# Optimization experiments

Measured on AMD Instinct MI355X. Metric: run time of the kernel, lower is better.

Reference implementation:

```python
import jax, jax.numpy as jnp
import numpy as np

B, L = 8192, 8192

def setup_inputs() -> dict:
    key = jax.random.key(0)
    ka, kb = jax.random.split(key)
    a = jax.random.normal(ka, (B, L), dtype=jnp.float32)
    b = jax.random.normal(kb, (B, L), dtype=jnp.float32)
    return {"a": a, "b": b}

def reference(a, b):
    # Original: (a[:, None, :] * b[:, :, None]).sum(-1)
    # out[n, i] = sum_j a[n, j] * b[n, i] = b[n, i] * sum_j a[n, j]
    # Algebraically identical, avoids the O(B*L*L) intermediate.
    return b * jnp.sum(a, axis=-1, keepdims=True)
```

## Files before the change

kernel.cpp:

```cpp
#include <hip/hip_runtime.h>


constexpr int L = 8192;
constexpr int BLOCK = 256;
constexpr int VEC_PER_THREAD = L / 4 / BLOCK;

__global__ __launch_bounds__(BLOCK) void outer_row_scale_kernel(
    const float* __restrict__ a,
    const float* __restrict__ b,
    float* __restrict__ out) {
    const size_t row = blockIdx.x;
    const float4* __restrict__ arow = reinterpret_cast<const float4*>(a + row * L);
    const float4* __restrict__ brow = reinterpret_cast<const float4*>(b + row * L);
    float4* __restrict__ orow = reinterpret_cast<float4*>(out + row * L);

    const int tid = threadIdx.x;

    float s = 0.0f;
    float4 va[VEC_PER_THREAD];
#pragma unroll
    for (int k = 0; k < VEC_PER_THREAD; ++k) {
        va[k] = arow[tid + k * BLOCK];
    }
#pragma unroll
    for (int k = 0; k < VEC_PER_THREAD; ++k) {
        s += (va[k].x + va[k].y) + (va[k].z + va[k].w);
    }

#pragma unroll
    for (int off = 32; off > 0; off >>= 1) {
        s += __shfl_down(s, off, 64);
    }

    __shared__ float wave_sums[BLOCK / 64];
    const int lane = tid & 63;
    const int wave = tid >> 6;
    if (lane == 0) wave_sums[wave] = s;
    __syncthreads();

    const float total = (wave_sums[0] + wave_sums[1]) + (wave_sums[2] + wave_sums[3]);

#pragma unroll
    for (int k = 0; k < VEC_PER_THREAD; ++k) {
        float4 vb = brow[tid + k * BLOCK];
        float4 vo;
        vo.x = vb.x * total;
        vo.y = vb.y * total;
        vo.z = vb.z * total;
        vo.w = vb.w * total;
        orow[tid + k * BLOCK] = vo;
    }
}

extern "C" void kernel_launch(void* const* d_in, const int* in_sizes, int n_in,
                              void* d_out, int out_size, void* d_ws, size_t ws_size,
                              hipStream_t stream) {
    const float* a = (const float*)d_in[0];
    const float* b = (const float*)d_in[1];
    float* out = (float*)d_out;
    const int B = in_sizes[0] / L;
    outer_row_scale_kernel<<<B, BLOCK, 0, stream>>>(a, b, out);
}
```

Baseline: 583.1 us.

## Split row-sum and scaling into two kernels using workspace

Splits the fused kernel into a row-sum kernel that writes per-row sums to workspace and a scale kernel that streams b and writes out, four rows per block. The aim is to take the reduction barrier out of the streaming pass so loads of b and stores of out are not held behind the sum of a. In exchange it adds a second launch and a small round-trip through global memory. The original fused kernel is kept as a fallback when the workspace is too small.

```diff
diff --git a/kernel.cpp b/kernel.cpp
--- a/kernel.cpp
+++ b/kernel.cpp
@@ -3,27 +3,24 @@
 
 constexpr int L = 8192;
 constexpr int BLOCK = 256;
-constexpr int VEC_PER_THREAD = L / 4 / BLOCK;
+constexpr int VEC = L / 4 / BLOCK;
+constexpr int ROWS_PER_BLOCK = 4;
 
-__global__ __launch_bounds__(BLOCK) void outer_row_scale_kernel(
-    const float* __restrict__ a,
-    const float* __restrict__ b,
-    float* __restrict__ out) {
+__global__ __launch_bounds__(BLOCK) void rowsum_kernel(
+    const float* __restrict__ a, float* __restrict__ sums) {
     const size_t row = blockIdx.x;
-    const float4* __restrict__ arow = reinterpret_cast<const float4*>(a + row * L);
-    const float4* __restrict__ brow = reinterpret_cast<const float4*>(b + row * L);
-    float4* __restrict__ orow = reinterpret_cast<float4*>(out + row * L);
-
+    const float4* __restrict__ arow =
+        reinterpret_cast<const float4*>(a + row * (size_t)L);
     const int tid = threadIdx.x;
 
-    float s = 0.0f;
-    float4 va[VEC_PER_THREAD];
+    float4 va[VEC];
 #pragma unroll
-    for (int k = 0; k < VEC_PER_THREAD; ++k) {
+    for (int k = 0; k < VEC; ++k) {
         va[k] = arow[tid + k * BLOCK];
     }
+    float s = 0.0f;
 #pragma unroll
-    for (int k = 0; k < VEC_PER_THREAD; ++k) {
+    for (int k = 0; k < VEC; ++k) {
         s += (va[k].x + va[k].y) + (va[k].z + va[k].w);
     }
 
@@ -38,10 +35,78 @@
     if (lane == 0) wave_sums[wave] = s;
     __syncthreads();
 
+    if (tid == 0) {
+        sums[row] = (wave_sums[0] + wave_sums[1]) + (wave_sums[2] + wave_sums[3]);
+    }
+}
+
+__global__ __launch_bounds__(BLOCK) void scale_kernel(
+    const float* __restrict__ b, const float* __restrict__ sums,
+    float* __restrict__ out) {
+    const size_t row0 = (size_t)blockIdx.x * ROWS_PER_BLOCK;
+    const int tid = threadIdx.x;
+
+    float s[ROWS_PER_BLOCK];
+#pragma unroll
+    for (int r = 0; r < ROWS_PER_BLOCK; ++r) {
+        s[r] = sums[row0 + r];
+    }
+
+#pragma unroll
+    for (int r = 0; r < ROWS_PER_BLOCK; ++r) {
+        const size_t row = row0 + r;
+        const float4* __restrict__ brow =
+            reinterpret_cast<const float4*>(b + row * (size_t)L);
+        float4* __restrict__ orow =
+            reinterpret_cast<float4*>(out + row * (size_t)L);
+        const float sr = s[r];
+#pragma unroll
+        for (int k = 0; k < VEC; ++k) {
+            float4 v = brow[tid + k * BLOCK];
+            v.x *= sr;
+            v.y *= sr;
+            v.z *= sr;
+            v.w *= sr;
+            orow[tid + k * BLOCK] = v;
+        }
+    }
+}
+
+__global__ __launch_bounds__(BLOCK) void outer_row_scale_kernel(
+    const float* __restrict__ a,
+    const float* __restrict__ b,
+    float* __restrict__ out) {
+    const size_t row = blockIdx.x;
+    const float4* __restrict__ arow = reinterpret_cast<const float4*>(a + row * (size_t)L);
+    const float4* __restrict__ brow = reinterpret_cast<const float4*>(b + row * (size_t)L);
+    float4* __restrict__ orow = reinterpret_cast<float4*>(out + row * (size_t)L);
+
+    const int tid = threadIdx.x;
+
+    float s = 0.0f;
+    float4 va[VEC];
+#pragma unroll
+    for (int k = 0; k < VEC; ++k) {
+        va[k] = arow[tid + k * BLOCK];
+    }
+#pragma unroll
+    for (int k = 0; k < VEC; ++k) {
+        s += (va[k].x + va[k].y) + (va[k].z + va[k].w);
+    }
+#pragma unroll
+    for (int off = 32; off > 0; off >>= 1) {
+        s += __shfl_down(s, off, 64);
+    }
+    __shared__ float wave_sums[BLOCK / 64];
+    const int lane = tid & 63;
+    const int wave = tid >> 6;
+    if (lane == 0) wave_sums[wave] = s;
+    __syncthreads();
+
     const float total = (wave_sums[0] + wave_sums[1]) + (wave_sums[2] + wave_sums[3]);
 
 #pragma unroll
-    for (int k = 0; k < VEC_PER_THREAD; ++k) {
+    for (int k = 0; k < VEC; ++k) {
         float4 vb = brow[tid + k * BLOCK];
         float4 vo;
         vo.x = vb.x * total;
@@ -59,5 +124,12 @@
     const float* b = (const float*)d_in[1];
     float* out = (float*)d_out;
     const int B = in_sizes[0] / L;
-    outer_row_scale_kernel<<<B, BLOCK, 0, stream>>>(a, b, out);
+
+    if (ws_size >= (size_t)B * sizeof(float)) {
+        float* sums = (float*)d_ws;
+        rowsum_kernel<<<B, BLOCK, 0, stream>>>(a, sums);
+        scale_kernel<<<B / ROWS_PER_BLOCK, BLOCK, 0, stream>>>(b, sums, out);
+    } else {
+        outer_row_scale_kernel<<<B, BLOCK, 0, stream>>>(a, b, out);
+    }
 }
```

Measured after the change: 583.8 us. About the same (+0.1%).

## Split into wave-per-row rowsum kernel and grid-stride nontemporal scale kernel

Applied to the files above, without the earlier changes.

Replaces the single fused kernel with two launches when workspace is available. The first computes the row sums of `a`, one wave per row, into a workspace buffer. The second streams `b` through a persistent grid-stride loop, scales each row and writes the output with nontemporal stores. The intent is higher memory-level parallelism and less cache pollution from the output writes, at the cost of an extra launch, a round trip for the sums, and no overlap between reading `a` and reading `b` within a block.

```diff
diff --git a/kernel.cpp b/kernel.cpp
--- a/kernel.cpp
+++ b/kernel.cpp
@@ -3,35 +3,91 @@
 
 constexpr int L = 8192;
 constexpr int BLOCK = 256;
-constexpr int VEC_PER_THREAD = L / 4 / BLOCK;
+constexpr int L4 = L / 4;
+constexpr int WAVES = BLOCK / 64;
+constexpr int F4_PER_LANE = L4 / 64;
+constexpr int VEC = L4 / BLOCK;
+
+typedef float fx4 __attribute__((ext_vector_type(4)));
+
+__global__ __launch_bounds__(BLOCK) void rowsum_kernel(
+    const float* __restrict__ a, float* __restrict__ sums) {
+    const int wave = threadIdx.x >> 6;
+    const int lane = threadIdx.x & 63;
+    const size_t row = (size_t)blockIdx.x * WAVES + wave;
+    const fx4* __restrict__ arow =
+        reinterpret_cast<const fx4*>(a + row * (size_t)L);
+
+    float p0 = 0.0f, p1 = 0.0f, p2 = 0.0f, p3 = 0.0f;
+#pragma unroll
+    for (int k = 0; k < F4_PER_LANE; k += 4) {
+        fx4 v0 = arow[lane + (k + 0) * 64];
+        fx4 v1 = arow[lane + (k + 1) * 64];
+        fx4 v2 = arow[lane + (k + 2) * 64];
+        fx4 v3 = arow[lane + (k + 3) * 64];
+        p0 += (v0.x + v0.y) + (v0.z + v0.w);
+        p1 += (v1.x + v1.y) + (v1.z + v1.w);
+        p2 += (v2.x + v2.y) + (v2.z + v2.w);
+        p3 += (v3.x + v3.y) + (v3.z + v3.w);
+    }
+    float s = (p0 + p1) + (p2 + p3);
+
+#pragma unroll
+    for (int off = 32; off > 0; off >>= 1) {
+        s += __shfl_down(s, off, 64);
+    }
+    if (lane == 0) sums[row] = s;
+}
+
+__global__ __launch_bounds__(BLOCK) void scale_kernel(
+    const float* __restrict__ b, const float* __restrict__ sums,
+    float* __restrict__ out, int nrows) {
+    const int tid = threadIdx.x;
+    int row = blockIdx.x;
+    float sr = sums[row];
+    for (; row < nrows; row += gridDim.x) {
+        const int next = row + gridDim.x;
+        const float sn = (next < nrows) ? sums[next] : 0.0f;
+
+        const fx4* __restrict__ brow =
+            reinterpret_cast<const fx4*>(b + (size_t)row * (size_t)L);
+        fx4* __restrict__ orow =
+            reinterpret_cast<fx4*>(out + (size_t)row * (size_t)L);
+#pragma unroll
+        for (int k = 0; k < VEC; ++k) {
+            fx4 v = brow[tid + k * BLOCK];
+            v *= sr;
+            __builtin_nontemporal_store(v, &orow[tid + k * BLOCK]);
+        }
+        sr = sn;
+    }
+}
 
 __global__ __launch_bounds__(BLOCK) void outer_row_scale_kernel(
     const float* __restrict__ a,
     const float* __restrict__ b,
     float* __restrict__ out) {
     const size_t row = blockIdx.x;
-    const float4* __restrict__ arow = reinterpret_cast<const float4*>(a + row * L);
-    const float4* __restrict__ brow = reinterpret_cast<const float4*>(b + row * L);
-    float4* __restrict__ orow = reinterpret_cast<float4*>(out + row * L);
+    const float4* __restrict__ arow = reinterpret_cast<const float4*>(a + row * (size_t)L);
+    const float4* __restrict__ brow = reinterpret_cast<const float4*>(b + row * (size_t)L);
+    float4* __restrict__ orow = reinterpret_cast<float4*>(out + row * (size_t)L);
 
     const int tid = threadIdx.x;
 
     float s = 0.0f;
-    float4 va[VEC_PER_THREAD];
+    float4 va[VEC];
 #pragma unroll
-    for (int k = 0; k < VEC_PER_THREAD; ++k) {
+    for (int k = 0; k < VEC; ++k) {
         va[k] = arow[tid + k * BLOCK];
     }
 #pragma unroll
-    for (int k = 0; k < VEC_PER_THREAD; ++k) {
+    for (int k = 0; k < VEC; ++k) {
         s += (va[k].x + va[k].y) + (va[k].z + va[k].w);
     }
-
 #pragma unroll
     for (int off = 32; off > 0; off >>= 1) {
         s += __shfl_down(s, off, 64);
     }
-
     __shared__ float wave_sums[BLOCK / 64];
     const int lane = tid & 63;
     const int wave = tid >> 6;
@@ -41,7 +97,7 @@
     const float total = (wave_sums[0] + wave_sums[1]) + (wave_sums[2] + wave_sums[3]);
 
 #pragma unroll
-    for (int k = 0; k < VEC_PER_THREAD; ++k) {
+    for (int k = 0; k < VEC; ++k) {
         float4 vb = brow[tid + k * BLOCK];
         float4 vo;
         vo.x = vb.x * total;
@@ -59,5 +115,13 @@
     const float* b = (const float*)d_in[1];
     float* out = (float*)d_out;
     const int B = in_sizes[0] / L;
-    outer_row_scale_kernel<<<B, BLOCK, 0, stream>>>(a, b, out);
+
+    if (ws_size >= (size_t)B * sizeof(float)) {
+        float* sums = (float*)d_ws;
+        rowsum_kernel<<<B / WAVES, BLOCK, 0, stream>>>(a, sums);
+        const int grid2 = 2048;
+        scale_kernel<<<grid2, BLOCK, 0, stream>>>(b, sums, out, B);
+    } else {
+        outer_row_scale_kernel<<<B, BLOCK, 0, stream>>>(a, b, out);
+    }
 }
```

Result: no change. 578.3 us (-0.8%).
